# Optimization experiments

Hardware: AMD Instinct MI355X
Metric: run time of the kernel (lower is better)

Reference implementation:

```python
import jax, jax.numpy as jnp
import numpy as np

SCALE = 2
PAD = 4
EPS = 1e-5
K = 5
N, C, H, W = 4, 64, 128, 128


def _splits(a, s):
    # (..., W, H) -> (..., W/s, H/s, s*s), block decimation matching torch view/permute
    *lead, Wd, Hd = a.shape
    b = a.reshape(*lead, s, Wd // s, s, Hd // s)
    nl = len(lead)
    b = jnp.transpose(b, tuple(range(nl)) + (nl + 1, nl + 3, nl, nl + 2))
    return b.reshape(*lead, Wd // s, Hd // s, s * s)


def _p2o(psf, Hs, Ws):
    # PSF -> OTF: zero-pad, roll to center at origin, FFT
    kh, kw = psf.shape[-2], psf.shape[-1]
    otf = jnp.zeros(psf.shape[:-2] + (Hs, Ws), psf.dtype).at[..., :kh, :kw].set(psf)
    otf = jnp.roll(otf, (-(kh // 2), -(kw // 2)), axis=(-2, -1))
    return jnp.fft.fftn(otf, axes=(-2, -1))


def _upsample(x, s):
    # s-fold zero-filling upsampler (S^T y)
    n, c, h, w = x.shape
    return jnp.zeros((n, c, h * s, w * s), x.dtype).at[..., ::s, ::s].set(x)


def setup_inputs() -> dict:
    key = jax.random.key(0)
    kx, kw_, _ = jax.random.split(key, 3)
    x = jax.random.normal(kx, (N, C, H, W), dtype=jnp.float32)
    w_raw = jax.random.normal(kw_, (1, C, K, K), dtype=jnp.float32)
    weight = jax.nn.softmax(w_raw.reshape(1, C, -1), axis=-1).reshape(1, C, K, K)
    bias = jnp.zeros((1, C, 1, 1), dtype=jnp.float32)
    return {"x": x, "weight": weight, "bias": bias}


def reference(x, weight, bias):
    s = SCALE
    xp = jnp.pad(x, ((0, 0), (0, 0), (PAD, PAD), (PAD, PAD)), mode="wrap")  # circular
    biaseps = jax.nn.sigmoid(bias - 9.0) + EPS  # (1,C,1,1)
    _, _, h, w = xp.shape
    STy = _upsample(xp, s)  # zero-filled upsample
    # nearest-neighbor interpolate by integer factor s
    xn = jnp.repeat(jnp.repeat(xp, s, axis=-2), s, axis=-1)
    FB = _p2o(weight, h * s, w * s)           # (1,C,hs,ws) complex
    FBC = jnp.conj(FB)
    F2B = jnp.abs(FB) ** 2                     # real
    FBFy = FBC * jnp.fft.fftn(STy, axes=(-2, -1))
    FR = FBFy + jnp.fft.fftn(biaseps * xn, axes=(-2, -1))
    x1 = FB * FR
    FBR = jnp.mean(_splits(x1, s), axis=-1)    # (N,C,h,w) complex
    invW = jnp.mean(_splits(F2B, s), axis=-1)  # (1,C,h,w) real
    invWBR = FBR / (invW + biaseps)
    FCBinvWBR = FBC * jnp.tile(invWBR, (1, 1, s, s))
    FX = (FR - FCBinvWBR) / biaseps
    out = jnp.real(jnp.fft.ifftn(FX, axes=(-2, -1)))
    out = out[..., PAD * s:-PAD * s, PAD * s:-PAD * s]
    return out
```

## Files before the change

kernel.cpp:

```cpp
#include <hip/hip_runtime.h>
#include <math.h>


#define MDIM 136
#define RSC  70
#define HC   69
#define PLANE_HALF (MDIM*HC)
#define NPLANES 256
#define LDS_CPLX  (MDIM*RSC + MDIM)
#define LDS_CPLX2 (2*MDIM*RSC + MDIM)
#define PI_D 3.14159265358979323846
#define NTH 1024

__device__ __forceinline__ int slot136(int k) { return 17*(k & 7) + (k >> 3); }
__device__ __forceinline__ int slot68(int k)  { return 17*(k & 3) + (k >> 2); }

template<int DIR, class F>
__device__ __forceinline__ void dft17_sink(float2* z, int base, int stride, F f)
{
    constexpr float C17[9] = {1.f, 0.93247223f, 0.73900892f, 0.44573836f,
                              0.09226836f, -0.27366299f, -0.60263464f,
                              -0.85021714f, -0.98297310f};
    constexpr float S17[9] = {0.f, 0.36124167f, 0.67369564f, 0.89516329f,
                              0.99573418f, 0.96182564f, 0.79801723f,
                              0.52643216f, 0.18374952f};
    constexpr float d = (DIR > 0) ? 1.f : -1.f;
    float xr[17], xi[17];
#pragma unroll
    for (int n = 0; n < 17; n++) {
        float2 v = z[base + n*stride];
        xr[n] = v.x; xi[n] = v.y;
    }
    float ar[8], ai[8], br[8], bi[8];
#pragma unroll
    for (int n = 1; n <= 8; n++) {
        ar[n-1] = xr[n] + xr[17-n];  ai[n-1] = xi[n] + xi[17-n];
        br[n-1] = xr[n] - xr[17-n];  bi[n-1] = xi[n] - xi[17-n];
    }
    float s0r = xr[0], s0i = xi[0];
#pragma unroll
    for (int n = 0; n < 8; n++) { s0r += ar[n]; s0i += ai[n]; }
    f(0, s0r, s0i);
#pragma unroll
    for (int k = 1; k <= 8; k++) {
        float Pr = xr[0], Pi = xi[0], Qr = 0.f, Qi = 0.f;
#pragma unroll
        for (int n = 1; n <= 8; n++) {
            int m = (k*n) % 17;
            float cc = (m <= 8) ? C17[m] : C17[17-m];
            float ss = (m <= 8) ? S17[m] : -S17[17-m];
            Pr = fmaf(ar[n-1], cc, Pr);
            Pi = fmaf(ai[n-1], cc, Pi);
            Qr = fmaf(br[n-1], ss, Qr);
            Qi = fmaf(bi[n-1], ss, Qi);
        }
        f(k,    Pr - d*Qi, Pi + d*Qr);
        f(17-k, Pr + d*Qi, Pi - d*Qr);
    }
}

template<int DIR>
__device__ __forceinline__ void radix4_tw(float2* z, const float2* lut, int base, int n2,
                                          float2 Z0, float2 Z1, float2 Z2, float2 Z3)
{
    constexpr float d = (DIR > 0) ? 1.0f : -1.0f;
    float t0r = Z0.x+Z2.x, t0i = Z0.y+Z2.y;
    float t1r = Z0.x-Z2.x, t1i = Z0.y-Z2.y;
    float t2r = Z1.x+Z3.x, t2i = Z1.y+Z3.y;
    float t3r = Z1.x-Z3.x, t3i = Z1.y-Z3.y;
    float X0r = t0r+t2r,     X0i = t0i+t2i;
    float X2r = t0r-t2r,     X2i = t0i-t2i;
    float X1r = t1r - d*t3i, X1i = t1i + d*t3r;
    float X3r = t1r + d*t3i, X3i = t1i - d*t3r;
    z[base + n2] = make_float2(X0r, X0i);
    float2 w1 = lut[2*n2], w2 = lut[4*n2], w3 = lut[6*n2];
    z[base + 17 + n2] = make_float2(X1r*w1.x - X1i*w1.y, X1r*w1.y + X1i*w1.x);
    z[base + 34 + n2] = make_float2(X2r*w2.x - X2i*w2.y, X2r*w2.y + X2i*w2.x);
    z[base + 51 + n2] = make_float2(X3r*w3.x - X3i*w3.y, X3r*w3.y + X3i*w3.x);
}

template<int DIR>
__device__ __forceinline__ void fft136_s1_body(float2* z, const float2* lut,
                                               int c, int n2)
{
    constexpr float d = (DIR > 0) ? 1.0f : -1.0f;
    constexpr float C707 = 0.70710678118654752f;
    float xr[8], xi[8];
#pragma unroll
    for (int n1 = 0; n1 < 8; n1++) {
        float2 v = z[(17*n1 + n2)*RSC + c];
        xr[n1] = v.x; xi[n1] = v.y;
    }
    float e0r = xr[0]+xr[4], e0i = xi[0]+xi[4];
    float e1r = xr[0]-xr[4], e1i = xi[0]-xi[4];
    float o0r = xr[2]+xr[6], o0i = xi[2]+xi[6];
    float o1r = xr[2]-xr[6], o1i = xi[2]-xi[6];
    float E0r = e0r+o0r, E0i = e0i+o0i;
    float E2r = e0r-o0r, E2i = e0i-o0i;
    float E1r = e1r - d*o1i, E1i = e1i + d*o1r;
    float E3r = e1r + d*o1i, E3i = e1i - d*o1r;
    float f0r = xr[1]+xr[5], f0i = xi[1]+xi[5];
    float f1r = xr[1]-xr[5], f1i = xi[1]-xi[5];
    float h0r = xr[3]+xr[7], h0i = xi[3]+xi[7];
    float h1r = xr[3]-xr[7], h1i = xi[3]-xi[7];
    float O0r = f0r+h0r, O0i = f0i+h0i;
    float O2r = f0r-h0r, O2i = f0i-h0i;
    float O1r = f1r - d*h1i, O1i = f1i + d*h1r;
    float O3r = f1r + d*h1i, O3i = f1i - d*h1r;
    float t1r =  C707*(O1r - d*O1i), t1i = C707*(O1i + d*O1r);
    float t2r = -d*O2i,              t2i = d*O2r;
    float t3r = -C707*(O3r + d*O3i), t3i = C707*(d*O3r - O3i);
    float Xr[8], Xi[8];
    Xr[0]=E0r+O0r; Xi[0]=E0i+O0i;  Xr[4]=E0r-O0r; Xi[4]=E0i-O0i;
    Xr[1]=E1r+t1r; Xi[1]=E1i+t1i;  Xr[5]=E1r-t1r; Xi[5]=E1i-t1i;
    Xr[2]=E2r+t2r; Xi[2]=E2i+t2i;  Xr[6]=E2r-t2r; Xi[6]=E2i-t2i;
    Xr[3]=E3r+t3r; Xi[3]=E3i+t3i;  Xr[7]=E3r-t3r; Xi[7]=E3i-t3i;
    z[n2*RSC + c] = make_float2(Xr[0], Xi[0]);
    int ti = 0;
#pragma unroll
    for (int k1 = 1; k1 < 8; k1++) {
        ti += n2;
        float2 w = lut[ti];
        z[(17*k1 + n2)*RSC + c] = make_float2(Xr[k1]*w.x - Xi[k1]*w.y,
                                              Xr[k1]*w.y + Xi[k1]*w.x);
    }
}

template<int DIR>
__device__ void fft136_s1(float2* z, const float2* lut, int ncols, int tid)
{
    int c = tid / 17;
    int n2 = tid - c*17;
    for (int e = tid; e < ncols*17; e += NTH) {
        fft136_s1_body<DIR>(z, lut, c, n2);
        c += 60; n2 += 4; if (n2 >= 17) { n2 -= 17; c++; }
    }
}

template<int DIR>
__device__ void ct68_s1(float2* z, const float2* lut, int tid)
{
    int row = tid / 17;
    int n2  = tid - row*17;
    for (int e = tid; e < MDIM*17; e += NTH) {
        int base = row*RSC;
        float2 Z0 = z[base + n2];
        float2 Z1 = z[base + 17 + n2];
        float2 Z2 = z[base + 34 + n2];
        float2 Z3 = z[base + 51 + n2];
        radix4_tw<DIR>(z, lut, base, n2, Z0, Z1, Z2, Z3);
        row += 60; n2 += 4; if (n2 >= 17) { n2 -= 17; row++; }
    }
}

__device__ __forceinline__ float2 c2r_pack(float2 a, float2 b, float2 w)
{
    float Sr = a.x + b.x, Si = a.y - b.y;
    float Dr = a.x - b.x, Di = a.y + b.y;
    float Or = w.x*Dr - w.y*Di, Oi = w.x*Di + w.y*Dr;
    return make_float2(Sr - Oi, Si + Or);
}

__global__ __launch_bounds__(1024, 8) void fwd_kernel(const float* __restrict__ x,
                                                      float2* __restrict__ Xhat)
{
    extern __shared__ float2 zsm[];
    float2* z   = zsm;
    float2* lut = zsm + MDIM*RSC;
    const int tid = threadIdx.x;

    if (tid < MDIM) {
        float s, c; sincosf(-2.0f*(float)PI_D*(float)tid/136.0f, &s, &c);
        lut[tid] = make_float2(c, s);
    }
    const float* xp = x + (size_t)blockIdx.x * (128*128);
    {
        int i = tid / 68, n = tid - (tid/68)*68;
        for (int e = tid; e < MDIM*68; e += NTH) {
            int si = (i + 124) & 127;
            int j0 = (2*n + 124) & 127;
            z[i*RSC + n] = *reinterpret_cast<const float2*>(xp + si*128 + j0);
            i += 15; n += 4; if (n >= 68) { n -= 68; i++; }
        }
    }
    __syncthreads();
    ct68_s1<-1>(z, lut, tid);
    __syncthreads();
    if (tid < MDIM*4) {
        int row = tid >> 2, k1 = tid & 3;
        int base = row*RSC + 17*k1;
        dft17_sink<-1>(z, base, 1, [&](int k2, float re, float im) {
            z[base + k2] = make_float2(re, im);
        });
    }
    __syncthreads();
    {
        int row = tid / 35, k = tid - (tid/35)*35;
        for (int e = tid; e < MDIM*35; e += NTH) {
            int base = row*RSC;
            int sa = slot68(k);
            float2 Za = z[base+sa];
            float Zar = Za.x, Zai = Za.y;
            float Zbr, Zbi; int sb;
            if (k == 0) { Zbr = Zar; Zbi = Zai; sb = 68; }
            else {
                int kk = 68-k; sb = slot68(kk);
                float2 Zb = z[base+sb]; Zbr = Zb.x; Zbi = Zb.y;
            }
            float2 w = lut[k];
            float wc = w.x, ws = w.y;
            float Er = 0.5f*(Zar + Zbr), Ei = 0.5f*(Zai - Zbi);
            float Dr = 0.5f*(Zar - Zbr), Di = 0.5f*(Zai + Zbi);
            float Tr = wc*Dr - ws*Di, Ti = wc*Di + ws*Dr;
            z[base+sa] = make_float2(Er + Ti, Ei - Tr);
            float E2r = Er,  E2i = -Ei;
            float D2r = -Dr, D2i = Di;
            float w2c = -wc, w2s = ws;
            float T2r = w2c*D2r - w2s*D2i, T2i = w2c*D2i + w2s*D2r;
            z[base+sb] = make_float2(E2r + T2i, E2i - T2r);
            row += 29; k += 9; if (k >= 35) { k -= 35; row++; }
        }
    }
    __syncthreads();
    fft136_s1<-1>(z, lut, HC, tid);
    __syncthreads();
    if (tid < HC*8) {
        int c = tid >> 3, k1 = tid & 7;
        int base = 17*k1*RSC + c;
        dft17_sink<-1>(z, base, RSC, [&](int k2, float re, float im) {
            z[base + k2*RSC] = make_float2(re, im);
        });
    }
    __syncthreads();
    float2* outp = Xhat + (size_t)blockIdx.x * PLANE_HALF;
    {
        int g1 = tid / HC, g2 = tid - (tid/HC)*HC;
        for (int e = tid; e < PLANE_HALF; e += NTH) {
            int cq = (g2 == 68) ? 68 : slot68(g2);
            outp[e] = z[slot136(g1)*RSC + cq];
            g1 += 14; g2 += 58; if (g2 >= HC) { g2 -= HC; g1++; }
        }
    }
}

__global__ void prep_kernel(const float* __restrict__ weight,
                            const float* __restrict__ bias,
                            float2* __restrict__ Abuf)
{
    __shared__ double tabc[272], tabs[272];
    for (int t = threadIdx.x; t < 272; t += blockDim.x) {
        double s, c; sincos(-2.0*PI_D*(double)t/272.0, &s, &c);
        tabc[t] = c; tabs[t] = s;
    }
    __syncthreads();

    const int c     = blockIdx.x >> 3;
    const int chunk = blockIdx.x & 7;
    const float* wp = weight + c*25;
    double w[25];
#pragma unroll
    for (int i = 0; i < 25; i++) w[i] = (double)wp[i];
    const double r = 1.0/(1.0 + exp(9.0 - (double)bias[c])) + 1e-5;

    const int e_lo = chunk * 1173;
    const int e_hi = e_lo + 1173;
    for (int e = e_lo + (int)threadIdx.x; e < e_hi; e += blockDim.x) {
        int g1 = e / HC, g2 = e - g1*HC;
        double c1 = tabc[g1], s1 = tabs[g1];
        double c2 = tabc[g2], s2 = tabs[g2];
        double e1r[5], e1i[5], e2r[5], e2i[5];
        e1r[2]=1.0; e1i[2]=0.0; e1r[3]=c1; e1i[3]=s1;
        e1r[4]=c1*c1-s1*s1; e1i[4]=2.0*c1*s1;
        e1r[1]=c1; e1i[1]=-s1; e1r[0]=e1r[4]; e1i[0]=-e1i[4];
        e2r[2]=1.0; e2i[2]=0.0; e2r[3]=c2; e2i[3]=s2;
        e2r[4]=c2*c2-s2*s2; e2i[4]=2.0*c2*s2;
        e2r[1]=c2; e2i[1]=-s2; e2r[0]=e2r[4]; e2i[0]=-e2i[4];

        double R0r[5],R0i[5],R1r[5],R1i[5];
#pragma unroll
        for (int a = 0; a < 5; a++) {
            double r0r=0,r0i=0,r1r=0,r1i=0;
#pragma unroll
            for (int b = 0; b < 5; b++) {
                double wv = w[a*5+b];
                double pr = wv*e2r[b], pi = wv*e2i[b];
                r0r += pr; r0i += pi;
                if (b & 1) { r1r -= pr; r1i -= pi; } else { r1r += pr; r1i += pi; }
            }
            R0r[a]=r0r; R0i[a]=r0i; R1r[a]=r1r; R1i[a]=r1i;
        }
        double FBr[2][2], FBi[2][2];
#pragma unroll
        for (int a1 = 0; a1 < 2; a1++)
#pragma unroll
            for (int b1 = 0; b1 < 2; b1++) {
                double fr=0, fi=0;
#pragma unroll
                for (int a = 0; a < 5; a++) {
                    double er = e1r[a], ei = e1i[a];
                    if (a1 && (a & 1)) { er = -er; ei = -ei; }
                    double Rr = b1 ? R1r[a] : R0r[a];
                    double Ri = b1 ? R1i[a] : R0i[a];
                    fr += er*Rr - ei*Ri;
                    fi += er*Ri + ei*Rr;
                }
                FBr[a1][b1]=fr; FBi[a1][b1]=fi;
            }
        double ur[2]={1.0+c1, 1.0-c1}, ui[2]={s1, -s1};
        double vr[2]={1.0+c2, 1.0-c2}, vi[2]={s2, -s2};
        double Br_[2][2], Bi_[2][2];
#pragma unroll
        for (int a1 = 0; a1 < 2; a1++)
#pragma unroll
            for (int b1 = 0; b1 < 2; b1++) {
                Br_[a1][b1] = ur[a1]*vr[b1] - ui[a1]*vi[b1];
                Bi_[a1][b1] = ur[a1]*vi[b1] + ui[a1]*vr[b1];
            }
        double invW=0, Qr=0, Qi=0;
#pragma unroll
        for (int a1 = 0; a1 < 2; a1++)
#pragma unroll
            for (int b1 = 0; b1 < 2; b1++) {
                invW += FBr[a1][b1]*FBr[a1][b1] + FBi[a1][b1]*FBi[a1][b1];
                Qr += FBr[a1][b1]*Br_[a1][b1] - FBi[a1][b1]*Bi_[a1][b1];
                Qi += FBr[a1][b1]*Bi_[a1][b1] + FBi[a1][b1]*Br_[a1][b1];
            }
        invW *= 0.25; Qr *= 0.25; Qi *= 0.25;
        double den = 1.0/(invW + r);
        double Sr = (1.0 - Qr)*den, Si = -Qi*den;
        double Mr[2][2], Mi[2][2];
#pragma unroll
        for (int a1 = 0; a1 < 2; a1++)
#pragma unroll
            for (int b1 = 0; b1 < 2; b1++) {
                Mr[a1][b1] = Br_[a1][b1] + FBr[a1][b1]*Sr + FBi[a1][b1]*Si;
                Mi[a1][b1] = Bi_[a1][b1] + FBr[a1][b1]*Si - FBi[a1][b1]*Sr;
            }
        const double scale = 1.0/73984.0;
#pragma unroll
        for (int uu = 0; uu < 2; uu++)
#pragma unroll
            for (int vv = 0; vv < 2; vv++) {
                double sr=0, si=0;
#pragma unroll
                for (int a1 = 0; a1 < 2; a1++)
#pragma unroll
                    for (int b1 = 0; b1 < 2; b1++) {
                        if ((a1*uu + b1*vv) & 1) { sr -= Mr[a1][b1]; si -= Mi[a1][b1]; }
                        else                     { sr += Mr[a1][b1]; si += Mi[a1][b1]; }
                    }
                int t = g1*uu + g2*vv;
                double pc = tabc[t], ps = -tabs[t];
                float2 outv;
                outv.x = (float)((pc*sr - ps*si)*scale);
                outv.y = (float)((pc*si + ps*sr)*scale);
                Abuf[((size_t)(c*4 + uu*2 + vv))*PLANE_HALF + e] = outv;
            }
    }
}

__global__ __launch_bounds__(1024, 4) void inv_kernel(const float2* __restrict__ Xhat,
                                                      const float2* __restrict__ Abuf,
                                                      float* __restrict__ out)
{
    extern __shared__ float2 zsm[];
    float2* z0  = zsm;
    float2* z1  = zsm + MDIM*RSC;
    float2* lut = zsm + 2*MDIM*RSC;
    const int tid = threadIdx.x;

    if (tid < MDIM) {
        float s, c; sincosf(2.0f*(float)PI_D*(float)tid/136.0f, &s, &c);
        lut[tid] = make_float2(c, s);
    }
    const int p  = blockIdx.x;
    const int u  = (p >> 3) & 1;
    const int nc = ((p >> 4) << 3) | (p & 7);
    const int c  = nc & 63;
    const float2* Xp  = Xhat + (size_t)nc * PLANE_HALF;
    const float2* Ap0 = Abuf + (size_t)(c*4 + u*2) * PLANE_HALF;
    const float2* Ap1 = Ap0 + PLANE_HALF;

    {
        int g1 = tid / HC, g2 = tid - (tid/HC)*HC;
        for (int e = tid; e < PLANE_HALF; e += NTH) {
            float2 xv = Xp[e], a0 = Ap0[e], a1 = Ap1[e];
            int a = g1*RSC + g2;
            z0[a] = make_float2(a0.x*xv.x - a0.y*xv.y, a0.x*xv.y + a0.y*xv.x);
            z1[a] = make_float2(a1.x*xv.x - a1.y*xv.y, a1.x*xv.y + a1.y*xv.x);
            g1 += 14; g2 += 58; if (g2 >= HC) { g2 -= HC; g1++; }
        }
    }
    __syncthreads();
    for (int it = tid; it < 2*HC*17; it += NTH) {
        int pl = it >= HC*17;
        int ee = it - (pl ? HC*17 : 0);
        int cc = (ee*241) >> 12;
        int n2 = ee - cc*17;
        fft136_s1_body<1>(pl ? z1 : z0, lut, cc, n2);
    }
    __syncthreads();
    for (int it = tid; it < 2*HC*8; it += NTH) {
        int pl = it >= HC*8;
        int i  = it - (pl ? HC*8 : 0);
        float2* zz = pl ? z1 : z0;
        int cc = i >> 3, k1 = i & 7;
        int base = 17*k1*RSC + cc;
        dft17_sink<1>(zz, base, RSC, [&](int k2, float re, float im) {
            zz[base + k2*RSC] = make_float2(re, im);
        });
    }
    __syncthreads();
    for (int it = tid; it < 2*MDIM*9; it += NTH) {
        int pl = it >= MDIM*9;
        int i  = it - (pl ? MDIM*9 : 0);
        float2* zz = pl ? z1 : z0;
        int row = (i*7282) >> 16;
        int g   = i - row*9;
        int base = row*RSC;
        if (g == 0) {
            float2 T0  = zz[base],    T17 = zz[base+17], T34 = zz[base+34],
                   T51 = zz[base+51], T68 = zz[base+68];
            float2 Z0 = c2r_pack(T0,  T68, lut[0]);
            float2 Z1 = c2r_pack(T17, T51, lut[17]);
            float2 Z2 = c2r_pack(T34, T34, lut[34]);
            float2 Z3 = c2r_pack(T51, T17, lut[51]);
            radix4_tw<1>(zz, lut, base, 0, Z0, Z1, Z2, Z3);
        } else {
            int gb = 17 - g;
            float2 Ta0 = zz[base+g],    Ta1 = zz[base+g+17],
                   Ta2 = zz[base+g+34], Ta3 = zz[base+g+51];
            float2 Tb0 = zz[base+gb],    Tb1 = zz[base+gb+17],
                   Tb2 = zz[base+gb+34], Tb3 = zz[base+gb+51];
            float2 Za0 = c2r_pack(Ta0, Tb3, lut[g]);
            float2 Za1 = c2r_pack(Ta1, Tb2, lut[g+17]);
            float2 Za2 = c2r_pack(Ta2, Tb1, lut[g+34]);
            float2 Za3 = c2r_pack(Ta3, Tb0, lut[g+51]);
            float2 Zb0 = c2r_pack(Tb0, Ta3, lut[gb]);
            float2 Zb1 = c2r_pack(Tb1, Ta2, lut[gb+17]);
            float2 Zb2 = c2r_pack(Tb2, Ta1, lut[gb+34]);
            float2 Zb3 = c2r_pack(Tb3, Ta0, lut[gb+51]);
            radix4_tw<1>(zz, lut, base, g,  Za0, Za1, Za2, Za3);
            radix4_tw<1>(zz, lut, base, gb, Zb0, Zb1, Zb2, Zb3);
        }
    }
    __syncthreads();
    for (int it = tid; it < 2*MDIM*4; it += NTH) {
        int pl = it >= MDIM*4;
        int i  = it - (pl ? MDIM*4 : 0);
        float2* zz = pl ? z1 : z0;
        int row = i >> 2, k1 = i & 3;
        int base = row*RSC + 17*k1;
        dft17_sink<1>(zz, base, 1, [&](int k2, float re, float im) {
            zz[base + k2] = make_float2(re, im);
        });
    }
    __syncthreads();
    float* op = out + (size_t)nc * (256*256);
    {
        int m  = 2 + (tid & 63);
        int y1 = 4 + (tid >> 6);
        int a  = slot136(y1)*RSC + slot68(m);
        float* rowp = op + (size_t)(2*y1 + u - 8)*256 + 4*m - 8;
#pragma unroll
        for (int it = 0; it < 8; ++it) {
            float2 w0 = z0[a], w1 = z1[a];
            *reinterpret_cast<float4*>(rowp) = make_float4(w0.x, w1.x, w0.y, w1.y);
            a += 2*RSC;
            rowp += 32*256;
        }
    }
}

extern "C" void kernel_launch(void* const* d_in, const int* in_sizes, int n_in,
                              void* d_out, int out_size, void* d_ws, size_t ws_size,
                              hipStream_t stream)
{
    const float* x      = (const float*)d_in[0];
    const float* weight = (const float*)d_in[1];
    const float* bias   = (const float*)d_in[2];
    float* out = (float*)d_out;

    float2* Xhat = (float2*)d_ws;
    float2* Abuf = Xhat + (size_t)NPLANES * PLANE_HALF;

    const size_t lds_fwd = (size_t)LDS_CPLX  * sizeof(float2);
    const size_t lds_inv = (size_t)LDS_CPLX2 * sizeof(float2);
    (void)hipFuncSetAttribute((const void*)fwd_kernel,
                              hipFuncAttributeMaxDynamicSharedMemorySize, (int)lds_fwd);
    (void)hipFuncSetAttribute((const void*)inv_kernel,
                              hipFuncAttributeMaxDynamicSharedMemorySize, (int)lds_inv);

    prep_kernel<<<512, 256, 0, stream>>>(weight, bias, Abuf);
    fwd_kernel<<<NPLANES, 1024, lds_fwd, stream>>>(x, Xhat);
    inv_kernel<<<NPLANES*2, 1024, lds_inv, stream>>>(Xhat, Abuf, out);
}
```

Baseline: 144.9 us.

## Fuse forward and inverse FFT kernels, keep spectrum in registers

Merges the forward FFT kernel and the inverse kernel into one conv_kernel per plane. The forward spectrum stays in registers and is reused for both output row parities in a serial loop, so the Xhat workspace round trip and one launch go away. The prep kernel also factors the 5x5 weight DFT, precomputing the column-direction partial sums in shared memory once per block. The cost is only 256 blocks of 1024 threads instead of 512 for the inverse stage, with the two u passes run serially inside each block, which lowers parallelism.

```diff
diff --git a/kernel.cpp b/kernel.cpp
--- a/kernel.cpp
+++ b/kernel.cpp
@@ -7,8 +7,7 @@
 #define HC   69
 #define PLANE_HALF (MDIM*HC)
 #define NPLANES 256
-#define LDS_CPLX  (MDIM*RSC + MDIM)
-#define LDS_CPLX2 (2*MDIM*RSC + MDIM)
+#define LDS_CPLX2 (2*MDIM*RSC + 2*MDIM)
 #define PI_D 3.14159265358979323846
 #define NTH 1024
 
@@ -161,36 +160,42 @@
     return make_float2(Sr - Oi, Si + Or);
 }
 
-__global__ __launch_bounds__(1024, 8) void fwd_kernel(const float* __restrict__ x,
-                                                      float2* __restrict__ Xhat)
+__global__ __launch_bounds__(1024, 4) void conv_kernel(const float* __restrict__ x,
+                                                       const float2* __restrict__ Abuf,
+                                                       float* __restrict__ out)
 {
     extern __shared__ float2 zsm[];
-    float2* z   = zsm;
-    float2* lut = zsm + MDIM*RSC;
+    float2* z0   = zsm;
+    float2* z1   = zsm + MDIM*RSC;
+    float2* lutI = zsm + 2*MDIM*RSC;
+    float2* lutF = lutI + MDIM;
     const int tid = threadIdx.x;
+    const int nc  = blockIdx.x;
+    const int c   = nc & 63;
 
     if (tid < MDIM) {
-        float s, c; sincosf(-2.0f*(float)PI_D*(float)tid/136.0f, &s, &c);
-        lut[tid] = make_float2(c, s);
-    }
-    const float* xp = x + (size_t)blockIdx.x * (128*128);
+        float s, cc; sincosf(2.0f*(float)PI_D*(float)tid/136.0f, &s, &cc);
+        lutI[tid] = make_float2(cc, s);
+        lutF[tid] = make_float2(cc, -s);
+    }
+    const float* xp = x + (size_t)nc * (128*128);
     {
         int i = tid / 68, n = tid - (tid/68)*68;
         for (int e = tid; e < MDIM*68; e += NTH) {
             int si = (i + 124) & 127;
             int j0 = (2*n + 124) & 127;
-            z[i*RSC + n] = *reinterpret_cast<const float2*>(xp + si*128 + j0);
+            z0[i*RSC + n] = *reinterpret_cast<const float2*>(xp + si*128 + j0);
             i += 15; n += 4; if (n >= 68) { n -= 68; i++; }
         }
     }
     __syncthreads();
-    ct68_s1<-1>(z, lut, tid);
+    ct68_s1<-1>(z0, lutF, tid);
     __syncthreads();
     if (tid < MDIM*4) {
         int row = tid >> 2, k1 = tid & 3;
         int base = row*RSC + 17*k1;
-        dft17_sink<-1>(z, base, 1, [&](int k2, float re, float im) {
-            z[base + k2] = make_float2(re, im);
+        dft17_sink<-1>(z0, base, 1, [&](int k2, float re, float im) {
+            z0[base + k2] = make_float2(re, im);
         });
     }
     __syncthreads();
@@ -199,47 +204,151 @@
         for (int e = tid; e < MDIM*35; e += NTH) {
             int base = row*RSC;
             int sa = slot68(k);
-            float2 Za = z[base+sa];
+            float2 Za = z0[base+sa];
             float Zar = Za.x, Zai = Za.y;
             float Zbr, Zbi; int sb;
             if (k == 0) { Zbr = Zar; Zbi = Zai; sb = 68; }
             else {
                 int kk = 68-k; sb = slot68(kk);
-                float2 Zb = z[base+sb]; Zbr = Zb.x; Zbi = Zb.y;
-            }
-            float2 w = lut[k];
+                float2 Zb = z0[base+sb]; Zbr = Zb.x; Zbi = Zb.y;
+            }
+            float2 w = lutF[k];
             float wc = w.x, ws = w.y;
             float Er = 0.5f*(Zar + Zbr), Ei = 0.5f*(Zai - Zbi);
             float Dr = 0.5f*(Zar - Zbr), Di = 0.5f*(Zai + Zbi);
             float Tr = wc*Dr - ws*Di, Ti = wc*Di + ws*Dr;
-            z[base+sa] = make_float2(Er + Ti, Ei - Tr);
+            z0[base+sa] = make_float2(Er + Ti, Ei - Tr);
             float E2r = Er,  E2i = -Ei;
             float D2r = -Dr, D2i = Di;
             float w2c = -wc, w2s = ws;
             float T2r = w2c*D2r - w2s*D2i, T2i = w2c*D2i + w2s*D2r;
-            z[base+sb] = make_float2(E2r + T2i, E2i - T2r);
+            z0[base+sb] = make_float2(E2r + T2i, E2i - T2r);
             row += 29; k += 9; if (k >= 35) { k -= 35; row++; }
         }
     }
     __syncthreads();
-    fft136_s1<-1>(z, lut, HC, tid);
+    fft136_s1<-1>(z0, lutF, HC, tid);
     __syncthreads();
     if (tid < HC*8) {
-        int c = tid >> 3, k1 = tid & 7;
-        int base = 17*k1*RSC + c;
-        dft17_sink<-1>(z, base, RSC, [&](int k2, float re, float im) {
-            z[base + k2*RSC] = make_float2(re, im);
+        int cc = tid >> 3, k1 = tid & 7;
+        int base = 17*k1*RSC + cc;
+        dft17_sink<-1>(z0, base, RSC, [&](int k2, float re, float im) {
+            z0[base + k2*RSC] = make_float2(re, im);
         });
     }
     __syncthreads();
-    float2* outp = Xhat + (size_t)blockIdx.x * PLANE_HALF;
+    float2 Xreg[10];
     {
         int g1 = tid / HC, g2 = tid - (tid/HC)*HC;
-        for (int e = tid; e < PLANE_HALF; e += NTH) {
-            int cq = (g2 == 68) ? 68 : slot68(g2);
-            outp[e] = z[slot136(g1)*RSC + cq];
+#pragma unroll
+        for (int k = 0; k < 10; k++) {
+            if (k < 9 || tid < PLANE_HALF - 9*NTH) {
+                int cq = (g2 == 68) ? 68 : slot68(g2);
+                Xreg[k] = z0[slot136(g1)*RSC + cq];
+            }
             g1 += 14; g2 += 58; if (g2 >= HC) { g2 -= HC; g1++; }
         }
+    }
+    __syncthreads();
+    float* op = out + (size_t)nc * (256*256);
+#pragma unroll 1
+    for (int u = 0; u < 2; u++) {
+        const float2* A0 = Abuf + (size_t)(c*4 + u*2) * PLANE_HALF;
+        const float2* A1 = A0 + PLANE_HALF;
+        {
+            int g1 = tid / HC, g2 = tid - (tid/HC)*HC;
+#pragma unroll
+            for (int k = 0; k < 10; k++) {
+                if (k < 9 || tid < PLANE_HALF - 9*NTH) {
+                    int e = tid + k*NTH;
+                    float2 xv = Xreg[k];
+                    float2 a0 = A0[e], a1 = A1[e];
+                    int a = g1*RSC + g2;
+                    z0[a] = make_float2(a0.x*xv.x - a0.y*xv.y, a0.x*xv.y + a0.y*xv.x);
+                    z1[a] = make_float2(a1.x*xv.x - a1.y*xv.y, a1.x*xv.y + a1.y*xv.x);
+                }
+                g1 += 14; g2 += 58; if (g2 >= HC) { g2 -= HC; g1++; }
+            }
+        }
+        __syncthreads();
+        for (int it = tid; it < 2*HC*17; it += NTH) {
+            int pl = it >= HC*17;
+            int ee = it - (pl ? HC*17 : 0);
+            int cc = (ee*241) >> 12;
+            int n2 = ee - cc*17;
+            fft136_s1_body<1>(pl ? z1 : z0, lutI, cc, n2);
+        }
+        __syncthreads();
+        for (int it = tid; it < 2*HC*8; it += NTH) {
+            int pl = it >= HC*8;
+            int i  = it - (pl ? HC*8 : 0);
+            float2* zz = pl ? z1 : z0;
+            int cc = i >> 3, k1 = i & 7;
+            int base = 17*k1*RSC + cc;
+            dft17_sink<1>(zz, base, RSC, [&](int k2, float re, float im) {
+                zz[base + k2*RSC] = make_float2(re, im);
+            });
+        }
+        __syncthreads();
+        for (int it = tid; it < 2*MDIM*9; it += NTH) {
+            int pl = it >= MDIM*9;
+            int i  = it - (pl ? MDIM*9 : 0);
+            float2* zz = pl ? z1 : z0;
+            int row = (i*7282) >> 16;
+            int g   = i - row*9;
+            int base = row*RSC;
+            if (g == 0) {
+                float2 T0  = zz[base],    T17 = zz[base+17], T34 = zz[base+34],
+                       T51 = zz[base+51], T68 = zz[base+68];
+                float2 Z0 = c2r_pack(T0,  T68, lutI[0]);
+                float2 Z1 = c2r_pack(T17, T51, lutI[17]);
+                float2 Z2 = c2r_pack(T34, T34, lutI[34]);
+                float2 Z3 = c2r_pack(T51, T17, lutI[51]);
+                radix4_tw<1>(zz, lutI, base, 0, Z0, Z1, Z2, Z3);
+            } else {
+                int gb = 17 - g;
+                float2 Ta0 = zz[base+g],    Ta1 = zz[base+g+17],
+                       Ta2 = zz[base+g+34], Ta3 = zz[base+g+51];
+                float2 Tb0 = zz[base+gb],    Tb1 = zz[base+gb+17],
+                       Tb2 = zz[base+gb+34], Tb3 = zz[base+gb+51];
+                float2 Za0 = c2r_pack(Ta0, Tb3, lutI[g]);
+                float2 Za1 = c2r_pack(Ta1, Tb2, lutI[g+17]);
+                float2 Za2 = c2r_pack(Ta2, Tb1, lutI[g+34]);
+                float2 Za3 = c2r_pack(Ta3, Tb0, lutI[g+51]);
+                float2 Zb0 = c2r_pack(Tb0, Ta3, lutI[gb]);
+                float2 Zb1 = c2r_pack(Tb1, Ta2, lutI[gb+17]);
+                float2 Zb2 = c2r_pack(Tb2, Ta1, lutI[gb+34]);
+                float2 Zb3 = c2r_pack(Tb3, Ta0, lutI[gb+51]);
+                radix4_tw<1>(zz, lutI, base, g,  Za0, Za1, Za2, Za3);
+                radix4_tw<1>(zz, lutI, base, gb, Zb0, Zb1, Zb2, Zb3);
+            }
+        }
+        __syncthreads();
+        for (int it = tid; it < 2*MDIM*4; it += NTH) {
+            int pl = it >= MDIM*4;
+            int i  = it - (pl ? MDIM*4 : 0);
+            float2* zz = pl ? z1 : z0;
+            int row = i >> 2, k1 = i & 3;
+            int base = row*RSC + 17*k1;
+            dft17_sink<1>(zz, base, 1, [&](int k2, float re, float im) {
+                zz[base + k2] = make_float2(re, im);
+            });
+        }
+        __syncthreads();
+        {
+            int m  = 2 + (tid & 63);
+            int y1 = 4 + (tid >> 6);
+            int a  = slot136(y1)*RSC + slot68(m);
+            float* rowp = op + (size_t)(2*y1 + u - 8)*256 + 4*m - 8;
+#pragma unroll
+            for (int it = 0; it < 8; ++it) {
+                float2 w0 = z0[a], w1 = z1[a];
+                *reinterpret_cast<float4*>(rowp) = make_float4(w0.x, w1.x, w0.y, w1.y);
+                a += 2*RSC;
+                rowp += 32*256;
+            }
+        }
+        __syncthreads();
     }
 }
 
@@ -248,64 +357,60 @@
                             float2* __restrict__ Abuf)
 {
     __shared__ double tabc[272], tabs[272];
+    __shared__ double Rs[69*5*4];
     for (int t = threadIdx.x; t < 272; t += blockDim.x) {
         double s, c; sincos(-2.0*PI_D*(double)t/272.0, &s, &c);
         tabc[t] = c; tabs[t] = s;
     }
-    __syncthreads();
-
     const int c     = blockIdx.x >> 3;
     const int chunk = blockIdx.x & 7;
     const float* wp = weight + c*25;
-    double w[25];
-#pragma unroll
-    for (int i = 0; i < 25; i++) w[i] = (double)wp[i];
     const double r = 1.0/(1.0 + exp(9.0 - (double)bias[c])) + 1e-5;
+    __syncthreads();
+    for (int it = threadIdx.x; it < 69*5; it += blockDim.x) {
+        int g2 = it / 5, a = it - 5*g2;
+        double c2 = tabc[g2], s2 = tabs[g2];
+        double e2r[5], e2i[5];
+        e2r[2]=1.0; e2i[2]=0.0; e2r[3]=c2; e2i[3]=s2;
+        e2r[4]=c2*c2-s2*s2; e2i[4]=2.0*c2*s2;
+        e2r[1]=c2; e2i[1]=-s2; e2r[0]=e2r[4]; e2i[0]=-e2i[4];
+        double w0=wp[a*5+0], w1=wp[a*5+1], w2=wp[a*5+2], w3=wp[a*5+3], w4=wp[a*5+4];
+        double Rer = w0*e2r[0] + w2*e2r[2] + w4*e2r[4];
+        double Rei = w0*e2i[0] + w2*e2i[2] + w4*e2i[4];
+        double Ror = w1*e2r[1] + w3*e2r[3];
+        double Roi = w1*e2i[1] + w3*e2i[3];
+        Rs[it*4+0] = Rer + Ror;  Rs[it*4+1] = Rei + Roi;
+        Rs[it*4+2] = Rer - Ror;  Rs[it*4+3] = Rei - Roi;
+    }
+    __syncthreads();
 
     const int e_lo = chunk * 1173;
     const int e_hi = e_lo + 1173;
-    for (int e = e_lo + (int)threadIdx.x; e < e_hi; e += blockDim.x) {
-        int g1 = e / HC, g2 = e - g1*HC;
+    int e  = e_lo + (int)threadIdx.x;
+    int g1 = e / HC, g2 = e - (e/HC)*HC;
+    for (; e < e_hi; e += blockDim.x) {
         double c1 = tabc[g1], s1 = tabs[g1];
-        double c2 = tabc[g2], s2 = tabs[g2];
-        double e1r[5], e1i[5], e2r[5], e2i[5];
+        double e1r[5], e1i[5];
         e1r[2]=1.0; e1i[2]=0.0; e1r[3]=c1; e1i[3]=s1;
         e1r[4]=c1*c1-s1*s1; e1i[4]=2.0*c1*s1;
         e1r[1]=c1; e1i[1]=-s1; e1r[0]=e1r[4]; e1i[0]=-e1i[4];
-        e2r[2]=1.0; e2i[2]=0.0; e2r[3]=c2; e2i[3]=s2;
-        e2r[4]=c2*c2-s2*s2; e2i[4]=2.0*c2*s2;
-        e2r[1]=c2; e2i[1]=-s2; e2r[0]=e2r[4]; e2i[0]=-e2i[4];
-
-        double R0r[5],R0i[5],R1r[5],R1i[5];
-#pragma unroll
-        for (int a = 0; a < 5; a++) {
-            double r0r=0,r0i=0,r1r=0,r1i=0;
-#pragma unroll
-            for (int b = 0; b < 5; b++) {
-                double wv = w[a*5+b];
-                double pr = wv*e2r[b], pi = wv*e2i[b];
-                r0r += pr; r0i += pi;
-                if (b & 1) { r1r -= pr; r1i -= pi; } else { r1r += pr; r1i += pi; }
-            }
-            R0r[a]=r0r; R0i[a]=r0i; R1r[a]=r1r; R1i[a]=r1i;
-        }
+
         double FBr[2][2], FBi[2][2];
 #pragma unroll
-        for (int a1 = 0; a1 < 2; a1++)
-#pragma unroll
-            for (int b1 = 0; b1 < 2; b1++) {
-                double fr=0, fi=0;
-#pragma unroll
-                for (int a = 0; a < 5; a++) {
-                    double er = e1r[a], ei = e1i[a];
-                    if (a1 && (a & 1)) { er = -er; ei = -ei; }
-                    double Rr = b1 ? R1r[a] : R0r[a];
-                    double Ri = b1 ? R1i[a] : R0i[a];
-                    fr += er*Rr - ei*Ri;
-                    fi += er*Ri + ei*Rr;
-                }
-                FBr[a1][b1]=fr; FBi[a1][b1]=fi;
-            }
+        for (int b1 = 0; b1 < 2; b1++) {
+            double Per=0, Pei=0, Por=0, Poi=0;
+#pragma unroll
+            for (int a = 0; a < 5; a++) {
+                double Rr = Rs[(g2*5+a)*4 + 2*b1];
+                double Ri = Rs[(g2*5+a)*4 + 2*b1 + 1];
+                double tr = e1r[a]*Rr - e1i[a]*Ri;
+                double ti = e1r[a]*Ri + e1i[a]*Rr;
+                if (a & 1) { Por += tr; Poi += ti; } else { Per += tr; Pei += ti; }
+            }
+            FBr[0][b1] = Per + Por;  FBi[0][b1] = Pei + Poi;
+            FBr[1][b1] = Per - Por;  FBi[1][b1] = Pei - Poi;
+        }
+        double c2 = tabc[g2], s2 = tabs[g2];
         double ur[2]={1.0+c1, 1.0-c1}, ui[2]={s1, -s1};
         double vr[2]={1.0+c2, 1.0-c2}, vi[2]={s2, -s2};
         double Br_[2][2], Bi_[2][2];
@@ -356,119 +461,7 @@
                 outv.y = (float)((pc*si + ps*sr)*scale);
                 Abuf[((size_t)(c*4 + uu*2 + vv))*PLANE_HALF + e] = outv;
             }
-    }
-}
-
-__global__ __launch_bounds__(1024, 4) void inv_kernel(const float2* __restrict__ Xhat,
-                                                      const float2* __restrict__ Abuf,
-                                                      float* __restrict__ out)
-{
-    extern __shared__ float2 zsm[];
-    float2* z0  = zsm;
-    float2* z1  = zsm + MDIM*RSC;
-    float2* lut = zsm + 2*MDIM*RSC;
-    const int tid = threadIdx.x;
-
-    if (tid < MDIM) {
-        float s, c; sincosf(2.0f*(float)PI_D*(float)tid/136.0f, &s, &c);
-        lut[tid] = make_float2(c, s);
-    }
-    const int p  = blockIdx.x;
-    const int u  = (p >> 3) & 1;
-    const int nc = ((p >> 4) << 3) | (p & 7);
-    const int c  = nc & 63;
-    const float2* Xp  = Xhat + (size_t)nc * PLANE_HALF;
-    const float2* Ap0 = Abuf + (size_t)(c*4 + u*2) * PLANE_HALF;
-    const float2* Ap1 = Ap0 + PLANE_HALF;
-
-    {
-        int g1 = tid / HC, g2 = tid - (tid/HC)*HC;
-        for (int e = tid; e < PLANE_HALF; e += NTH) {
-            float2 xv = Xp[e], a0 = Ap0[e], a1 = Ap1[e];
-            int a = g1*RSC + g2;
-            z0[a] = make_float2(a0.x*xv.x - a0.y*xv.y, a0.x*xv.y + a0.y*xv.x);
-            z1[a] = make_float2(a1.x*xv.x - a1.y*xv.y, a1.x*xv.y + a1.y*xv.x);
-            g1 += 14; g2 += 58; if (g2 >= HC) { g2 -= HC; g1++; }
-        }
-    }
-    __syncthreads();
-    for (int it = tid; it < 2*HC*17; it += NTH) {
-        int pl = it >= HC*17;
-        int ee = it - (pl ? HC*17 : 0);
-        int cc = (ee*241) >> 12;
-        int n2 = ee - cc*17;
-        fft136_s1_body<1>(pl ? z1 : z0, lut, cc, n2);
-    }
-    __syncthreads();
-    for (int it = tid; it < 2*HC*8; it += NTH) {
-        int pl = it >= HC*8;
-        int i  = it - (pl ? HC*8 : 0);
-        float2* zz = pl ? z1 : z0;
-        int cc = i >> 3, k1 = i & 7;
-        int base = 17*k1*RSC + cc;
-        dft17_sink<1>(zz, base, RSC, [&](int k2, float re, float im) {
-            zz[base + k2*RSC] = make_float2(re, im);
-        });
-    }
-    __syncthreads();
-    for (int it = tid; it < 2*MDIM*9; it += NTH) {
-        int pl = it >= MDIM*9;
-        int i  = it - (pl ? MDIM*9 : 0);
-        float2* zz = pl ? z1 : z0;
-        int row = (i*7282) >> 16;
-        int g   = i - row*9;
-        int base = row*RSC;
-        if (g == 0) {
-            float2 T0  = zz[base],    T17 = zz[base+17], T34 = zz[base+34],
-                   T51 = zz[base+51], T68 = zz[base+68];
-            float2 Z0 = c2r_pack(T0,  T68, lut[0]);
-            float2 Z1 = c2r_pack(T17, T51, lut[17]);
-            float2 Z2 = c2r_pack(T34, T34, lut[34]);
-            float2 Z3 = c2r_pack(T51, T17, lut[51]);
-            radix4_tw<1>(zz, lut, base, 0, Z0, Z1, Z2, Z3);
-        } else {
-            int gb = 17 - g;
-            float2 Ta0 = zz[base+g],    Ta1 = zz[base+g+17],
-                   Ta2 = zz[base+g+34], Ta3 = zz[base+g+51];
-            float2 Tb0 = zz[base+gb],    Tb1 = zz[base+gb+17],
-                   Tb2 = zz[base+gb+34], Tb3 = zz[base+gb+51];
-            float2 Za0 = c2r_pack(Ta0, Tb3, lut[g]);
-            float2 Za1 = c2r_pack(Ta1, Tb2, lut[g+17]);
-            float2 Za2 = c2r_pack(Ta2, Tb1, lut[g+34]);
-            float2 Za3 = c2r_pack(Ta3, Tb0, lut[g+51]);
-            float2 Zb0 = c2r_pack(Tb0, Ta3, lut[gb]);
-            float2 Zb1 = c2r_pack(Tb1, Ta2, lut[gb+17]);
-            float2 Zb2 = c2r_pack(Tb2, Ta1, lut[gb+34]);
-            float2 Zb3 = c2r_pack(Tb3, Ta0, lut[gb+51]);
-            radix4_tw<1>(zz, lut, base, g,  Za0, Za1, Za2, Za3);
-            radix4_tw<1>(zz, lut, base, gb, Zb0, Zb1, Zb2, Zb3);
-        }
-    }
-    __syncthreads();
-    for (int it = tid; it < 2*MDIM*4; it += NTH) {
-        int pl = it >= MDIM*4;
-        int i  = it - (pl ? MDIM*4 : 0);
-        float2* zz = pl ? z1 : z0;
-        int row = i >> 2, k1 = i & 3;
-        int base = row*RSC + 17*k1;
-        dft17_sink<1>(zz, base, 1, [&](int k2, float re, float im) {
-            zz[base + k2] = make_float2(re, im);
-        });
-    }
-    __syncthreads();
-    float* op = out + (size_t)nc * (256*256);
-    {
-        int m  = 2 + (tid & 63);
-        int y1 = 4 + (tid >> 6);
-        int a  = slot136(y1)*RSC + slot68(m);
-        float* rowp = op + (size_t)(2*y1 + u - 8)*256 + 4*m - 8;
-#pragma unroll
-        for (int it = 0; it < 8; ++it) {
-            float2 w0 = z0[a], w1 = z1[a];
-            *reinterpret_cast<float4*>(rowp) = make_float4(w0.x, w1.x, w0.y, w1.y);
-            a += 2*RSC;
-            rowp += 32*256;
-        }
+        g1 += 3; g2 += 49; if (g2 >= HC) { g2 -= HC; g1++; }
     }
 }
 
@@ -481,17 +474,12 @@
     const float* bias   = (const float*)d_in[2];
     float* out = (float*)d_out;
 
-    float2* Xhat = (float2*)d_ws;
-    float2* Abuf = Xhat + (size_t)NPLANES * PLANE_HALF;
-
-    const size_t lds_fwd = (size_t)LDS_CPLX  * sizeof(float2);
-    const size_t lds_inv = (size_t)LDS_CPLX2 * sizeof(float2);
-    (void)hipFuncSetAttribute((const void*)fwd_kernel,
-                              hipFuncAttributeMaxDynamicSharedMemorySize, (int)lds_fwd);
-    (void)hipFuncSetAttribute((const void*)inv_kernel,
-                              hipFuncAttributeMaxDynamicSharedMemorySize, (int)lds_inv);
+    float2* Abuf = (float2*)d_ws;
+
+    const size_t lds_conv = (size_t)LDS_CPLX2 * sizeof(float2);
+    (void)hipFuncSetAttribute((const void*)conv_kernel,
+                              hipFuncAttributeMaxDynamicSharedMemorySize, (int)lds_conv);
 
     prep_kernel<<<512, 256, 0, stream>>>(weight, bias, Abuf);
-    fwd_kernel<<<NPLANES, 1024, lds_fwd, stream>>>(x, Xhat);
-    inv_kernel<<<NPLANES*2, 1024, lds_inv, stream>>>(Xhat, Abuf, out);
-}
+    conv_kernel<<<NPLANES, 1024, lds_conv, stream>>>(x, Abuf, out);
+}
```

New measurement: 140.7 us. 1.03x faster.
